# Kernel optimization log

Hardware: AMD Instinct MI355X
Metric: run time of the kernel (lower is better)

The kernel has to match this reference:

```python
import jax, jax.numpy as jnp
import numpy as np

OUT_H, OUT_W = 32, 256  # hardcoded output grid in the original call()


def setup_inputs() -> dict:
    key = jax.random.key(0)
    k1, k2 = jax.random.split(key)
    img = jax.random.uniform(k1, (256, 512), dtype=jnp.float32)
    # fractional offset guarantees (i+pos0-ii)^2 + (j+pos1-ij)^2 > 0 everywhere
    pos = jax.random.uniform(k2, (2,), dtype=jnp.float32) * 8.0 + 0.3
    return {"img": img, "pos": pos}


def reference(img, pos):
    # r[i, j] = sum_{ii, ij} img[ii, ij] / ((i + pos0 - ii)^2 + (j + pos1 - ij)^2)
    H, W = img.shape
    ii = jnp.arange(H, dtype=img.dtype)
    ij = jnp.arange(W, dtype=img.dtype)
    j = jnp.arange(OUT_W, dtype=img.dtype)
    dy2 = (j[:, None] + pos[1] - ij[None, :]) ** 2  # [OUT_W, W]

    def row(carry, i):
        dx2 = (i + pos[0] - ii) ** 2                       # [H]
        w = 1.0 / (dx2[None, :, None] + dy2[:, None, :])   # [OUT_W, H, W]
        r_i = jnp.einsum('jhw,hw->j', w, img)              # [OUT_W]
        return carry, r_i

    i_vals = jnp.arange(OUT_H, dtype=img.dtype)
    _, r = jax.lax.scan(row, 0, i_vals)  # scan over 32 output rows keeps peak memory ~134 MB
    return r  # [OUT_H, OUT_W]
```

## Files before the change

### kernel.cpp

```cpp
#include <hip/hip_runtime.h>


constexpr int H  = 256;
constexpr int W  = 512;
constexpr int OH = 32;
constexpr int OW = 256;
constexpr int NR = 8;
constexpr int KROW = 800;
constexpr int BLK = 256;

__device__ __forceinline__ int swz(int x) {
    const int seg = x >> 5;
    const int off = x & 31;
    return (seg << 5) | ((off + ((seg & 7) << 2)) & 31);
}

__global__ __launch_bounds__(BLK, 4) void corr2(
    const float* __restrict__ img, const float* __restrict__ pos,
    float* __restrict__ out)
{
    __shared__ float Ks[NR * KROW];
    __shared__ float red[NR][OW];

    const int i   = blockIdx.x;
    const int ii0 = blockIdx.y * NR;
    const int tid = threadIdx.x;

    const float pos0 = pos[0];
    const float pos1 = pos[1];

    for (int rg = 0; rg < NR; ++rg) {
        const float dx  = (float)(i - (ii0 + rg)) + pos0;
        const float dx2 = dx * dx;
        for (int x = tid; x < KROW; x += BLK) {
            const float dy = (float)(x - 516) + pos1;
            Ks[rg * KROW + swz(x)] = 1.0f / (dx2 + dy * dy);
        }
    }
    __syncthreads();

    const int wv  = tid >> 6;
    const int L   = tid & 31;
    const int hf  = (tid >> 5) & 1;
    const int rg  = wv * 2 + hf;
    const int row = ii0 + rg;

    const float4* __restrict__ ip = (const float4*)(img + row * W);
    const int kbase = rg * KROW;

    float acc[8] = {0.f,0.f,0.f,0.f,0.f,0.f,0.f,0.f};

    int wq = 8 * L + 512;
    float4 qa = *(const float4*)&Ks[kbase + swz(wq)];
    float4 qb = *(const float4*)&Ks[kbase + swz(wq + 4)];
    float4 qc = *(const float4*)&Ks[kbase + swz(wq + 8)];

    int ci = 0;

#define STEP(Q0, Q1, Q2)                                                      \
    do {                                                                      \
        const float4 iv = ip[ci];                                             \
        _Pragma("unroll")                                                     \
        for (int p = 0; p < 8; ++p) {                                         \
            _Pragma("unroll")                                                 \
            for (int s = 0; s < 4; ++s) {                                     \
                const int d = p - s + 4;       \
                const float kv = (d < 4) ? ((const float*)&(Q0))[d]           \
                               : (d < 8) ? ((const float*)&(Q1))[d - 4]       \
                                         : ((const float*)&(Q2))[d - 8];      \
                acc[p] = fmaf(((const float*)&iv)[s], kv, acc[p]);            \
            }                                                                 \
        }                                                                     \
        wq -= 4; ++ci;                                                        \
                     \
        (Q2) = *(const float4*)&Ks[kbase + swz(wq)];                          \
    } while (0)

#pragma unroll 1
    for (int t = 0; t < 42; ++t) {
        STEP(qa, qb, qc);
        STEP(qc, qa, qb);
        STEP(qb, qc, qa);
    }
    STEP(qa, qb, qc);
    STEP(qc, qa, qb);
#undef STEP

#pragma unroll
    for (int p = 0; p < 8; ++p)
        red[rg][8 * L + p] = acc[p];
    __syncthreads();

    {
        const int j = tid;
        float s = 0.f;
#pragma unroll
        for (int r = 0; r < NR; ++r) s += red[r][j];
        atomicAdd(&out[i * OW + j], s);
    }
}

extern "C" void kernel_launch(void* const* d_in, const int* in_sizes, int n_in,
                              void* d_out, int out_size, void* d_ws, size_t ws_size,
                              hipStream_t stream) {
    const float* img = (const float*)d_in[0];
    const float* pos = (const float*)d_in[1];
    float* out = (float*)d_out;

    hipMemsetAsync(out, 0, (size_t)out_size * sizeof(float), stream);

    dim3 grid(OH, H / NR);
    corr2<<<grid, BLK, 0, stream>>>(img, pos, out);
}
```

Before: 91.02 us.

## Widen per-thread output tile to 16 columns and split image row halves

Each thread now computes 16 output columns instead of 8. Two thread groups split each image row into halves and their partial sums are combined with cross-lane shuffles before the shared-memory reduction. This gives more FMAs per loaded image and kernel value, which should reduce LDS and global load traffic per FLOP, and it halves the number of serial steps per thread. The cost is more registers (16 accumulators plus 8 float4 kernel windows), which may lower occupancy, and extra clamped loads at the boundaries.

```diff
diff --git a/kernel.cpp b/kernel.cpp
--- a/kernel.cpp
+++ b/kernel.cpp
@@ -5,9 +5,9 @@
 constexpr int W  = 512;
 constexpr int OH = 32;
 constexpr int OW = 256;
-constexpr int NR = 8;
+constexpr int NR   = 8;
 constexpr int KROW = 800;
-constexpr int BLK = 256;
+constexpr int BLK  = 256;
 
 __device__ __forceinline__ int swz(int x) {
     const int seg = x >> 5;
@@ -15,12 +15,37 @@
     return (seg << 5) | ((off + ((seg & 7) << 2)) & 31);
 }
 
-__global__ __launch_bounds__(BLK, 4) void corr2(
+__device__ __forceinline__ void step64(const float4 iv,
+    const float4 qa, const float4 qb, const float4 qc,
+    const float4 qd, const float4 qe, float* __restrict__ acc)
+{
+    const float* A = (const float*)&qa;
+    const float* Bq = (const float*)&qb;
+    const float* C = (const float*)&qc;
+    const float* D = (const float*)&qd;
+    const float* E = (const float*)&qe;
+    const float* I = (const float*)&iv;
+#pragma unroll
+    for (int p = 0; p < 16; ++p) {
+#pragma unroll
+        for (int s = 0; s < 4; ++s) {
+            const int k = p - s + 4;
+            const float kv = (k < 4)  ? E[k]
+                           : (k < 8)  ? D[k - 4]
+                           : (k < 12) ? C[k - 8]
+                           : (k < 16) ? Bq[k - 12]
+                                      : A[k - 16];
+            acc[p] = fmaf(I[s], kv, acc[p]);
+        }
+    }
+}
+
+__global__ __launch_bounds__(BLK, 4) void corr3(
     const float* __restrict__ img, const float* __restrict__ pos,
     float* __restrict__ out)
 {
     __shared__ float Ks[NR * KROW];
-    __shared__ float red[NR][OW];
+    __shared__ float red[4][OW];
 
     const int i   = blockIdx.x;
     const int ii0 = blockIdx.y * NR;
@@ -33,69 +58,80 @@
         const float dx  = (float)(i - (ii0 + rg)) + pos0;
         const float dx2 = dx * dx;
         for (int x = tid; x < KROW; x += BLK) {
-            const float dy = (float)(x - 516) + pos1;
+            const float dy = (float)(x - 512) + pos1;
             Ks[rg * KROW + swz(x)] = 1.0f / (dx2 + dy * dy);
         }
     }
     __syncthreads();
 
-    const int wv  = tid >> 6;
-    const int L   = tid & 31;
-    const int hf  = (tid >> 5) & 1;
-    const int rg  = wv * 2 + hf;
+    const int M  = tid & 15;
+    const int G  = tid >> 4;
+    const int rg = G >> 1;
+    const int h  = G & 1;
     const int row = ii0 + rg;
 
-    const float4* __restrict__ ip = (const float4*)(img + row * W);
-    const int kbase = rg * KROW;
+    const float*  kb = &Ks[rg * KROW];
+    const float4* ip = (const float4*)(img + row * W + 256 * h);
 
-    float acc[8] = {0.f,0.f,0.f,0.f,0.f,0.f,0.f,0.f};
+    const int B0 = 16 * M + 512 - 256 * h;
 
-    int wq = 8 * L + 512;
-    float4 qa = *(const float4*)&Ks[kbase + swz(wq)];
-    float4 qb = *(const float4*)&Ks[kbase + swz(wq + 4)];
-    float4 qc = *(const float4*)&Ks[kbase + swz(wq + 8)];
+    float4 Q0 = *(const float4*)&kb[swz(B0 + 12)];
+    float4 Q1 = *(const float4*)&kb[swz(B0 +  8)];
+    float4 Q2 = *(const float4*)&kb[swz(B0 +  4)];
+    float4 Q3 = *(const float4*)&kb[swz(B0     )];
+    float4 Q4 = *(const float4*)&kb[swz(B0 -  4)];
+    float4 Q5 = *(const float4*)&kb[swz(B0 -  8)];
+    float4 Q6 = *(const float4*)&kb[swz(B0 - 12)];
+    float4 Q7;
 
-    int ci = 0;
+    float acc[16];
+#pragma unroll
+    for (int p = 0; p < 16; ++p) acc[p] = 0.f;
 
-#define STEP(Q0, Q1, Q2)                                                      \
+    float4 ivA = ip[0], ivB;
+    int wrd = B0 - 16;
+    int ci  = 0;
+
+#define S1(QA, QB, QC, QD, QE, QT, IVC, IVN)                                  \
     do {                                                                      \
-        const float4 iv = ip[ci];                                             \
-        _Pragma("unroll")                                                     \
-        for (int p = 0; p < 8; ++p) {                                         \
-            _Pragma("unroll")                                                 \
-            for (int s = 0; s < 4; ++s) {                                     \
-                const int d = p - s + 4;       \
-                const float kv = (d < 4) ? ((const float*)&(Q0))[d]           \
-                               : (d < 8) ? ((const float*)&(Q1))[d - 4]       \
-                                         : ((const float*)&(Q2))[d - 8];      \
-                acc[p] = fmaf(((const float*)&iv)[s], kv, acc[p]);            \
-            }                                                                 \
-        }                                                                     \
-        wq -= 4; ++ci;                                                        \
-                     \
-        (Q2) = *(const float4*)&Ks[kbase + swz(wq)];                          \
+        IVN = ip[ci < 63 ? ci + 1 : 63];                                      \
+        const int trc = wrd > 0 ? wrd : 0;                                    \
+        QT = *(const float4*)&kb[swz(trc)];                                   \
+        wrd -= 4;                                                             \
+        step64(IVC, QA, QB, QC, QD, QE, acc);                                 \
+        ++ci;                                                                 \
     } while (0)
 
 #pragma unroll 1
-    for (int t = 0; t < 42; ++t) {
-        STEP(qa, qb, qc);
-        STEP(qc, qa, qb);
-        STEP(qb, qc, qa);
+    for (int t8 = 0; t8 < 8; ++t8) {
+        S1(Q0, Q1, Q2, Q3, Q4, Q7, ivA, ivB);
+        S1(Q1, Q2, Q3, Q4, Q5, Q0, ivB, ivA);
+        S1(Q2, Q3, Q4, Q5, Q6, Q1, ivA, ivB);
+        S1(Q3, Q4, Q5, Q6, Q7, Q2, ivB, ivA);
+        S1(Q4, Q5, Q6, Q7, Q0, Q3, ivA, ivB);
+        S1(Q5, Q6, Q7, Q0, Q1, Q4, ivB, ivA);
+        S1(Q6, Q7, Q0, Q1, Q2, Q5, ivA, ivB);
+        S1(Q7, Q0, Q1, Q2, Q3, Q6, ivB, ivA);
     }
-    STEP(qa, qb, qc);
-    STEP(qc, qa, qb);
-#undef STEP
+#undef S1
 
 #pragma unroll
-    for (int p = 0; p < 8; ++p)
-        red[rg][8 * L + p] = acc[p];
+    for (int p = 0; p < 16; ++p) {
+        acc[p] += __shfl_xor(acc[p], 16);
+        acc[p] += __shfl_xor(acc[p], 32);
+    }
+
+    const int wv = tid >> 6;
+    if ((tid & 48) == 0) {
+#pragma unroll
+        for (int p = 0; p < 16; ++p)
+            red[wv][16 * M + p] = acc[p];
+    }
     __syncthreads();
 
     {
         const int j = tid;
-        float s = 0.f;
-#pragma unroll
-        for (int r = 0; r < NR; ++r) s += red[r][j];
+        const float s = red[0][j] + red[1][j] + red[2][j] + red[3][j];
         atomicAdd(&out[i * OW + j], s);
     }
 }
@@ -110,5 +146,5 @@
     hipMemsetAsync(out, 0, (size_t)out_size * sizeof(float), stream);
 
     dim3 grid(OH, H / NR);
-    corr2<<<grid, BLK, 0, stream>>>(img, pos, out);
+    corr3<<<grid, BLK, 0, stream>>>(img, pos, out);
 }
```

Measured after the change: 87.58 us. 1.04x faster.
